# Optimization experiments

Measured on AMD Instinct MI355X. Metric: run time of the kernel, lower is better.

Reference implementation:

```python
import jax, jax.numpy as jnp
import numpy as np

N_NODES = 100000
N_EDGES = 3200000
IN_FEATS = 512
EDGE_FEATS = 24
OUT_FEATS = 512
LN_EPS = 1e-5


def setup_inputs() -> dict:
    key = jax.random.key(0)
    ks = jax.random.split(key, 8)
    h = jax.random.normal(ks[0], (N_NODES, IN_FEATS), dtype=jnp.float32)
    m = jax.random.normal(ks[1], (N_EDGES, EDGE_FEATS), dtype=jnp.float32)
    dst = jax.random.randint(ks[2], (N_EDGES,), 0, N_NODES, dtype=jnp.int32)
    norm = jax.random.uniform(ks[3], (N_NODES, 1), dtype=jnp.float32)
    stdv = 1.0 / np.sqrt(IN_FEATS + EDGE_FEATS)
    W = jax.random.uniform(ks[4], (OUT_FEATS, IN_FEATS + EDGE_FEATS), dtype=jnp.float32, minval=-stdv, maxval=stdv)
    b = jax.random.uniform(ks[5], (OUT_FEATS,), dtype=jnp.float32, minval=-stdv, maxval=stdv)
    gamma = jnp.ones((OUT_FEATS,), dtype=jnp.float32)
    beta = jnp.zeros((OUT_FEATS,), dtype=jnp.float32)
    return {"h": h, "m": m, "dst": dst, "norm": norm, "W": W, "b": b, "gamma": gamma, "beta": beta}


def reference(h, m, dst, norm, W, b, gamma, beta):
    # copy_e + sum: segment-sum edge features into destination nodes -> [N, 24]
    ah = jax.ops.segment_sum(m, dst, num_segments=N_NODES)
    # scale by per-node norm, concat with node features -> [N, in+24]
    x = jnp.concatenate([h, ah * norm], axis=1)
    # linear
    y = jnp.einsum('nd,od->no', x, W) + b
    # layernorm (elementwise affine)
    mu = jnp.mean(y, axis=-1, keepdims=True)
    var = jnp.mean((y - mu) ** 2, axis=-1, keepdims=True)
    y = gamma * (y - mu) * jax.lax.rsqrt(var + LN_EPS) + beta
    # activation = relu
    return jax.nn.relu(y)
```

## Files before the change

### kernel.cpp

```cpp
#include <hip/hip_runtime.h>
#include <hip/hip_bf16.h>
#include <stdint.h>

#define NN 100000
#define NE 3200000
#define EF 24
#define KF 536
#define BM 64
#define GSTRIDE 25
#define NGEMM 1563
#define NSCAT 37500
#define NBLK (NGEMM + NSCAT)

typedef __attribute__((ext_vector_type(8))) short bf16x8;
typedef __attribute__((ext_vector_type(8))) unsigned short u16x8;
typedef __attribute__((ext_vector_type(4))) float f32x4;

__device__ __forceinline__ unsigned short f2bf(float f) {
  union { float f; unsigned int u; } v; v.f = f;
  unsigned int r = v.u + 0x7FFFu + ((v.u >> 16) & 1u);
  return (unsigned short)(r >> 16);
}

__device__ __forceinline__ void gload_lds16(const void* g, void* l) {
  __builtin_amdgcn_global_load_lds(
      (const __attribute__((address_space(1))) unsigned int*)g,
      (__attribute__((address_space(3))) unsigned int*)l, 16, 0, 0);
}

__global__ void wconv_kernel(const float* __restrict__ W, unsigned short* __restrict__ Wb) {
  int i = blockIdx.x * blockDim.x + threadIdx.x;
  if (i >= 17 * 32 * 64 * 8) return;
  int j = i & 7;
  int lane = (i >> 3) & 63;
  int nt = (i >> 9) & 31;
  int kt = i >> 14;
  int row = nt * 16 + (lane & 15);
  int k = kt * 32 + (lane >> 4) * 8 + j;
  float v = (k < KF) ? W[row * KF + k] : 0.0f;
  Wb[i] = f2bf(v);
}

__global__ __launch_bounds__(256) void init_u64_kernel(unsigned long long* __restrict__ acc) {
  int i = blockIdx.x * 256 + threadIdx.x;
  if (i < NN * 6) acc[i] = 0x4000400040004000ULL;
}

__global__ __launch_bounds__(512, 4) void fusedA_kernel(
    const float* __restrict__ h, const float* __restrict__ m,
    const int* __restrict__ dst, const unsigned short* __restrict__ Wb,
    unsigned long long* __restrict__ acc, float* __restrict__ out) {
  __shared__ __align__(16) unsigned short Alds[2 * 2048];
  __shared__ __align__(16) unsigned short Blds[2 * 16384];

  const int bid = blockIdx.x;
  const int t = threadIdx.x;

  if (bid % GSTRIDE != 0) {
    int sidx = bid - bid / GSTRIDE - 1;
    int i = sidx * 512 + t;
    int e = i / 6;
    int fp = i - e * 6;
    float4 v = *(const float4*)(m + (size_t)e * EF + fp * 4);
    long long a0 = (long long)__float2int_rn(v.x * 128.f);
    long long a1 = (long long)__float2int_rn(v.y * 128.f);
    long long a2 = (long long)__float2int_rn(v.z * 128.f);
    long long a3 = (long long)__float2int_rn(v.w * 128.f);
    unsigned long long add = (unsigned long long)(a0 + (a1 << 16) + (a2 << 32) + (a3 << 48));
    atomicAdd(acc + (size_t)dst[e] * 6 + fp, add);
    return;
  }

  const int g = bid / GSTRIDE;
  const int lane = t & 63;
  const int w = t >> 6;
  const int lgrp = lane >> 4;
  const int llow = lane & 15;
  const int mg = w >> 2;
  const int ng = w & 3;
  const int blockRow = g * BM;

  const int am = t >> 3;
  const int c = t & 7;
  const int kkw = c >> 2;
  const int akg = c & 3;
  const int arow = blockRow + am;
  char* aldsdst = (char*)Alds + kkw * 4096 + (((am >> 4) * 64 + akg * 16 + (am & 15)) * 16);

  f32x4 acc2[2][8];
#pragma unroll
  for (int i = 0; i < 2; ++i)
#pragma unroll
    for (int j = 0; j < 8; ++j) acc2[i][j] = (f32x4){0.f, 0.f, 0.f, 0.f};

  float4 ra0 = make_float4(0.f, 0.f, 0.f, 0.f), ra1 = ra0;
  if (arow < NN) {
    const float* p = h + (size_t)arow * 512 + c * 8;
    ra0 = *(const float4*)p;
    ra1 = *(const float4*)(p + 4);
  }

  for (int step = 0; step < 8; ++step) {
#pragma unroll
    for (int kk = 0; kk < 2; ++kk) {
      const unsigned short* src = Wb + ((size_t)((step * 2 + kk) * 32 + w) * 64 + lane) * 8;
#pragma unroll
      for (int j = 0; j < 4; ++j)
        gload_lds16(src + (size_t)j * 8 * 64 * 8, (char*)Blds + kk * 32768 + (j * 8 + w) * 1024);
    }
    {
      u16x8 bv;
      bv[0] = f2bf(ra0.x); bv[1] = f2bf(ra0.y); bv[2] = f2bf(ra0.z); bv[3] = f2bf(ra0.w);
      bv[4] = f2bf(ra1.x); bv[5] = f2bf(ra1.y); bv[6] = f2bf(ra1.z); bv[7] = f2bf(ra1.w);
      *(u16x8*)aldsdst = bv;
    }
    ra0 = make_float4(0.f, 0.f, 0.f, 0.f); ra1 = ra0;
    if (step < 7 && arow < NN) {
      const float* p = h + (size_t)arow * 512 + (step + 1) * 64 + c * 8;
      ra0 = *(const float4*)p;
      ra1 = *(const float4*)(p + 4);
    }
    __syncthreads();

#pragma unroll
    for (int kk = 0; kk < 2; ++kk) {
      bf16x8 af0 = *(const bf16x8*)((const char*)Alds + kk * 4096 + (((mg * 2 + 0) * 64) + lane) * 16);
      bf16x8 af1 = *(const bf16x8*)((const char*)Alds + kk * 4096 + (((mg * 2 + 1) * 64) + lane) * 16);
#pragma unroll
      for (int j = 0; j < 8; ++j) {
        int nt = ng * 8 + j;
        bf16x8 bf = *(const bf16x8*)((const char*)Blds + kk * 32768 + ((nt * 64) + lane) * 16);
        acc2[0][j] = __builtin_amdgcn_mfma_f32_16x16x32_bf16(af0, bf, acc2[0][j], 0, 0, 0);
        acc2[1][j] = __builtin_amdgcn_mfma_f32_16x16x32_bf16(af1, bf, acc2[1][j], 0, 0, 0);
      }
    }
    __syncthreads();
  }

#pragma unroll
  for (int mt = 0; mt < 2; ++mt) {
#pragma unroll
    for (int r = 0; r < 4; ++r) {
      int lrow = (mg * 2 + mt) * 16 + lgrp * 4 + r;
      int grow = blockRow + lrow;
      if (grow < NN) {
#pragma unroll
        for (int j = 0; j < 8; ++j) {
          int col = (ng * 8 + j) * 16 + llow;
          out[(size_t)grow * 512 + col] = acc2[mt][j][r];
        }
      }
    }
  }
}

__global__ __launch_bounds__(512, 4) void epilogue_kernel(
    const unsigned long long* __restrict__ acc, const float* __restrict__ norm,
    const unsigned short* __restrict__ Wb,
    const float* __restrict__ bias, const float* __restrict__ gamma,
    const float* __restrict__ beta, float* __restrict__ out) {
  __shared__ __align__(16) unsigned short Alds[2048];
  __shared__ __align__(16) unsigned short Blds[16384];
  __shared__ float red[4][BM][2];
  __shared__ float stats[BM][2];

  const int t = threadIdx.x;
  const int lane = t & 63;
  const int w = t >> 6;
  const int lgrp = lane >> 4;
  const int llow = lane & 15;
  const int mg = w >> 2;
  const int ng = w & 3;
  const int g = blockIdx.x;
  const int blockRow = g * BM;

  {
    const unsigned short* src = Wb + ((size_t)(16 * 32 + w) * 64 + lane) * 8;
#pragma unroll
    for (int j = 0; j < 4; ++j)
      gload_lds16(src + (size_t)j * 8 * 64 * 8, (char*)Blds + (j * 8 + w) * 1024);
  }
  if (t < 384) {
    int row = t / 6;
    int fp = t - row * 6;
    int nrow = blockRow + row;
    unsigned long long x = 0x4000400040004000ULL;
    float nv = 0.f;
    if (nrow < NN) {
      x = acc[(size_t)nrow * 6 + fp];
      nv = norm[nrow] * (1.0f / 128.0f);
    }
    ushort4 o;
    o.x = f2bf((float)((int)((x >> 0) & 0xFFFF) - 16384) * nv);
    o.y = f2bf((float)((int)((x >> 16) & 0xFFFF) - 16384) * nv);
    o.z = f2bf((float)((int)((x >> 32) & 0xFFFF) - 16384) * nv);
    o.w = f2bf((float)((int)((x >> 48) & 0xFFFF) - 16384) * nv);
    int akg = fp >> 1;
    int half = fp & 1;
    *(ushort4*)((char*)Alds + (((row >> 4) * 64 + akg * 16 + (row & 15)) * 16 + half * 8)) = o;
  } else {
    int tt = t - 384;
    int row = tt >> 1;
    int half = tt & 1;
    *(ushort4*)((char*)Alds + (((row >> 4) * 64 + 3 * 16 + (row & 15)) * 16 + half * 8)) =
        make_ushort4(0, 0, 0, 0);
  }
  __syncthreads();

  f32x4 acc2[2][8];
#pragma unroll
  for (int i = 0; i < 2; ++i)
#pragma unroll
    for (int j = 0; j < 8; ++j) acc2[i][j] = (f32x4){0.f, 0.f, 0.f, 0.f};
  {
    bf16x8 af0 = *(const bf16x8*)((const char*)Alds + (((mg * 2 + 0) * 64) + lane) * 16);
    bf16x8 af1 = *(const bf16x8*)((const char*)Alds + (((mg * 2 + 1) * 64) + lane) * 16);
#pragma unroll
    for (int j = 0; j < 8; ++j) {
      int nt = ng * 8 + j;
      bf16x8 bf = *(const bf16x8*)((const char*)Blds + ((nt * 64) + lane) * 16);
      acc2[0][j] = __builtin_amdgcn_mfma_f32_16x16x32_bf16(af0, bf, acc2[0][j], 0, 0, 0);
      acc2[1][j] = __builtin_amdgcn_mfma_f32_16x16x32_bf16(af1, bf, acc2[1][j], 0, 0, 0);
    }
  }

#pragma unroll
  for (int mt = 0; mt < 2; ++mt) {
#pragma unroll
    for (int r = 0; r < 4; ++r) {
      int lrow = (mg * 2 + mt) * 16 + lgrp * 4 + r;
      int grow = blockRow + lrow;
      if (grow < NN) {
#pragma unroll
        for (int j = 0; j < 8; ++j) {
          int col = (ng * 8 + j) * 16 + llow;
          acc2[mt][j][r] += out[(size_t)grow * 512 + col];
        }
      }
    }
  }

  float bcol[8], gcol[8], btcol[8];
#pragma unroll
  for (int j = 0; j < 8; ++j) {
    int col = (ng * 8 + j) * 16 + llow;
    bcol[j] = bias[col];
    gcol[j] = gamma[col];
    btcol[j] = beta[col];
  }
  float s[2][4], ss[2][4];
#pragma unroll
  for (int mt = 0; mt < 2; ++mt)
#pragma unroll
    for (int r = 0; r < 4; ++r) { s[mt][r] = 0.f; ss[mt][r] = 0.f; }
#pragma unroll
  for (int mt = 0; mt < 2; ++mt)
#pragma unroll
    for (int j = 0; j < 8; ++j)
#pragma unroll
      for (int r = 0; r < 4; ++r) {
        float v = acc2[mt][j][r] + bcol[j];
        acc2[mt][j][r] = v;
        s[mt][r] += v;
        ss[mt][r] += v * v;
      }
#pragma unroll
  for (int off = 1; off < 16; off <<= 1) {
#pragma unroll
    for (int mt = 0; mt < 2; ++mt)
#pragma unroll
      for (int r = 0; r < 4; ++r) {
        s[mt][r] += __shfl_xor(s[mt][r], off, 64);
        ss[mt][r] += __shfl_xor(ss[mt][r], off, 64);
      }
  }
  if (llow == 0) {
#pragma unroll
    for (int mt = 0; mt < 2; ++mt)
#pragma unroll
      for (int r = 0; r < 4; ++r) {
        int lrow = (mg * 2 + mt) * 16 + lgrp * 4 + r;
        red[ng][lrow][0] = s[mt][r];
        red[ng][lrow][1] = ss[mt][r];
      }
  }
  __syncthreads();
  if (t < BM) {
    float sum = red[0][t][0] + red[1][t][0] + red[2][t][0] + red[3][t][0];
    float sq = red[0][t][1] + red[1][t][1] + red[2][t][1] + red[3][t][1];
    float mean = sum * (1.0f / 512.0f);
    float var = sq * (1.0f / 512.0f) - mean * mean;
    stats[t][0] = mean;
    stats[t][1] = rsqrtf(var + 1e-5f);
  }
  __syncthreads();
#pragma unroll
  for (int mt = 0; mt < 2; ++mt) {
#pragma unroll
    for (int r = 0; r < 4; ++r) {
      int lrow = (mg * 2 + mt) * 16 + lgrp * 4 + r;
      int grow = blockRow + lrow;
      if (grow < NN) {
        float mean = stats[lrow][0];
        float rstd = stats[lrow][1];
#pragma unroll
        for (int j = 0; j < 8; ++j) {
          int col = (ng * 8 + j) * 16 + llow;
          float v = (acc2[mt][j][r] - mean) * rstd * gcol[j] + btcol[j];
          out[(size_t)grow * 512 + col] = fmaxf(v, 0.0f);
        }
      }
    }
  }
}

extern "C" void kernel_launch(void* const* d_in, const int* in_sizes, int n_in,
                              void* d_out, int out_size, void* d_ws, size_t ws_size,
                              hipStream_t stream) {
  const float* h = (const float*)d_in[0];
  const float* m = (const float*)d_in[1];
  const int* dst = (const int*)d_in[2];
  const float* norm = (const float*)d_in[3];
  const float* W = (const float*)d_in[4];
  const float* b = (const float*)d_in[5];
  const float* gamma = (const float*)d_in[6];
  const float* beta = (const float*)d_in[7];
  float* out = (float*)d_out;

  unsigned short* Wb = (unsigned short*)d_ws;
  unsigned long long* acc = (unsigned long long*)((char*)d_ws + 1048576);

  init_u64_kernel<<<(NN * 6 + 255) / 256, 256, 0, stream>>>(acc);
  wconv_kernel<<<(17 * 32 * 64 * 8 + 255) / 256, 256, 0, stream>>>(W, Wb);
  fusedA_kernel<<<NBLK, 512, 0, stream>>>(h, m, dst, Wb, acc, out);
  epilogue_kernel<<<NGEMM, 512, 0, stream>>>(acc, norm, Wb, b, gamma, beta, out);
}
```

Baseline: 387.8 us.

## Stage GEMM partials in a thread-native blocked layout with vectorized stores

```diff
diff --git a/kernel.cpp b/kernel.cpp
--- a/kernel.cpp
+++ b/kernel.cpp
@@ -11,6 +11,7 @@
 #define NGEMM 1563
 #define NSCAT 37500
 #define NBLK (NGEMM + NSCAT)
+#define OUTB 204800000ULL
 
 typedef __attribute__((ext_vector_type(8))) short bf16x8;
 typedef __attribute__((ext_vector_type(8))) unsigned short u16x8;
@@ -74,18 +75,17 @@
   const int g = bid / GSTRIDE;
   const int lane = t & 63;
   const int w = t >> 6;
-  const int lgrp = lane >> 4;
-  const int llow = lane & 15;
   const int mg = w >> 2;
   const int ng = w & 3;
   const int blockRow = g * BM;
 
-  const int am = t >> 3;
-  const int c = t & 7;
-  const int kkw = c >> 2;
-  const int akg = c & 3;
-  const int arow = blockRow + am;
-  char* aldsdst = (char*)Alds + kkw * 4096 + (((am >> 4) * 64 + akg * 16 + (am & 15)) * 16);
+  const int kkA = t >> 8;
+  const int sA = t & 255;
+  const int rowA = ((sA >> 6) << 4) | (sA & 15);
+  const int akgA = (sA >> 4) & 3;
+  const int arow = blockRow + rowA;
+  char* aldsdst = (char*)Alds + kkA * 4096 + sA * 16;
+  const float* asrc = h + (size_t)arow * 512 + kkA * 32 + akgA * 8;
 
   f32x4 acc2[2][8];
 #pragma unroll
@@ -95,9 +95,8 @@
 
   float4 ra0 = make_float4(0.f, 0.f, 0.f, 0.f), ra1 = ra0;
   if (arow < NN) {
-    const float* p = h + (size_t)arow * 512 + c * 8;
-    ra0 = *(const float4*)p;
-    ra1 = *(const float4*)(p + 4);
+    ra0 = *(const float4*)asrc;
+    ra1 = *(const float4*)(asrc + 4);
   }
 
   for (int step = 0; step < 8; ++step) {
@@ -116,7 +115,7 @@
     }
     ra0 = make_float4(0.f, 0.f, 0.f, 0.f); ra1 = ra0;
     if (step < 7 && arow < NN) {
-      const float* p = h + (size_t)arow * 512 + (step + 1) * 64 + c * 8;
+      const float* p = asrc + (step + 1) * 64;
       ra0 = *(const float4*)p;
       ra1 = *(const float4*)(p + 4);
     }
@@ -137,20 +136,13 @@
     __syncthreads();
   }
 
-#pragma unroll
-  for (int mt = 0; mt < 2; ++mt) {
-#pragma unroll
-    for (int r = 0; r < 4; ++r) {
-      int lrow = (mg * 2 + mt) * 16 + lgrp * 4 + r;
-      int grow = blockRow + lrow;
-      if (grow < NN) {
-#pragma unroll
-        for (int j = 0; j < 8; ++j) {
-          int col = (ng * 8 + j) * 16 + llow;
-          out[(size_t)grow * 512 + col] = acc2[mt][j][r];
-        }
-      }
-    }
+  if ((size_t)g * 131072 + ((size_t)t + 1) * 256 <= OUTB) {
+    float* pp = out + (size_t)g * 32768 + (size_t)t * 64;
+#pragma unroll
+    for (int mt = 0; mt < 2; ++mt)
+#pragma unroll
+      for (int j = 0; j < 8; ++j)
+        *(f32x4*)(pp + (mt * 8 + j) * 4) = acc2[mt][j];
   }
 }
 
@@ -224,20 +216,18 @@
     }
   }
 
-#pragma unroll
-  for (int mt = 0; mt < 2; ++mt) {
-#pragma unroll
-    for (int r = 0; r < 4; ++r) {
-      int lrow = (mg * 2 + mt) * 16 + lgrp * 4 + r;
-      int grow = blockRow + lrow;
-      if (grow < NN) {
-#pragma unroll
-        for (int j = 0; j < 8; ++j) {
-          int col = (ng * 8 + j) * 16 + llow;
-          acc2[mt][j][r] += out[(size_t)grow * 512 + col];
-        }
-      }
-    }
+  if ((size_t)g * 131072 + ((size_t)t + 1) * 256 <= OUTB) {
+    const float* pp = out + (size_t)g * 32768 + (size_t)t * 64;
+#pragma unroll
+    for (int mt = 0; mt < 2; ++mt)
+#pragma unroll
+      for (int j = 0; j < 8; ++j) {
+        f32x4 q = *(const f32x4*)(pp + (mt * 8 + j) * 4);
+        acc2[mt][j][0] += q[0];
+        acc2[mt][j][1] += q[1];
+        acc2[mt][j][2] += q[2];
+        acc2[mt][j][3] += q[3];
+      }
   }
 
   float bcol[8], gcol[8], btcol[8];
```

Measured after the change: 399.4 us. +3.0%, slower.
